# Performance work log

Hardware: AMD Instinct MI355X
Metric: run time of the kernel (lower is better)

The kernel has to match this reference:

```python
import jax, jax.numpy as jnp
import numpy as np

NUM_POINTS = 1_000_000
WINDOW = 8                      # 2^3 corner stencil for linear shape functions in 3D
GRID = (128, 128, 128)
NUM_CELLS = GRID[0] * GRID[1] * GRID[2]
CELL = 1.0 / 64.0
INV_CELL = 64.0
ORIGIN = jnp.zeros((3,), dtype=jnp.float32)
# forward_window: the 8 corner offsets of the enclosing cell
FWD_WINDOW = jnp.array([[i, j, k] for i in (0, 1) for j in (0, 1) for k in (0, 1)],
                       dtype=jnp.int32)  # [8,3]


def setup_inputs() -> dict:
    key = jax.random.key(0)
    k1, k2, k3 = jax.random.split(key, 3)
    domain = GRID[0] * CELL
    # keep particles one cell away from the boundary so all stencil hashes are in range
    pos = jax.random.uniform(k1, (NUM_POINTS, 3), dtype=jnp.float32) * (domain - 2 * CELL) + CELL
    vel = jax.random.normal(k2, (NUM_POINTS, 3), dtype=jnp.float32)
    mass = jax.random.uniform(k3, (NUM_POINTS,), dtype=jnp.float32) * 1e-3 + 1e-4
    return {"position_stack": pos, "velocity_stack": vel, "mass_stack": mass}


def reference(position_stack, velocity_stack, mass_stack):
    # ---- get_interactions: gather particle pos, hash into grid, shape functions ----
    rel = (position_stack - ORIGIN) * INV_CELL               # [N,3] position in cell units
    base = jnp.floor(rel)                                    # [N,3]
    grid_pos = base[:, None, :] + FWD_WINDOW[None, :, :].astype(rel.dtype)  # [N,8,3]
    dist = rel[:, None, :] - grid_pos                        # [N,8,3], each dim in (-1,1)

    gp = grid_pos.astype(jnp.int32)
    # get_hash, dim==3: pos[2] + pos[0]*grid[2] + pos[1]*grid[2]*grid[0]
    intr_hash = gp[..., 2] + gp[..., 0] * GRID[2] + gp[..., 1] * (GRID[2] * GRID[0])  # [N,8]

    # linear shape function: N = prod_d (1 - |x_d|); grad scaled by inv_cell_size
    w = 1.0 - jnp.abs(dist)                                  # [N,8,3]
    shapef = w[..., 0] * w[..., 1] * w[..., 2]               # [N,8]
    valid = (intr_hash >= 0) & (intr_hash < NUM_CELLS)
    shapef = jnp.where(valid, shapef, 0.0)

    g0 = -jnp.sign(dist[..., 0]) * w[..., 1] * w[..., 2]
    g1 = -jnp.sign(dist[..., 1]) * w[..., 0] * w[..., 2]
    g2 = -jnp.sign(dist[..., 2]) * w[..., 0] * w[..., 1]
    shapef_grad = jnp.stack([g0, g1, g2], axis=-1) * INV_CELL  # [N,8,3]
    shapef_grad = jnp.where(valid[..., None], shapef_grad, 0.0)

    # intr_dist_padded = -dist * cell_size (kept implicitly via dist; used in APIC-style p2g)
    # ---- p2g scatter (vmap_intr_scatter semantics): mass & momentum to grid nodes ----
    h_flat = jnp.clip(intr_hash, 0, NUM_CELLS - 1).reshape(-1)  # [N*8]
    sm = shapef * mass_stack[:, None]                           # [N,8]
    node_mass = jax.ops.segment_sum(sm.reshape(-1), h_flat, num_segments=NUM_CELLS)   # [C]
    mom = sm[..., None] * velocity_stack[:, None, :]            # [N,8,3]
    node_mom = jax.ops.segment_sum(mom.reshape(-1, 3), h_flat, num_segments=NUM_CELLS)  # [C,3]

    return jnp.concatenate([node_mass[:, None], node_mom], axis=1)  # [C,4]
```

## Files before the change

### kernel.cpp

```cpp
#include <hip/hip_runtime.h>
#include <hip/hip_fp16.h>


#define GRID_DIM   128
#define NUM_CELLS  (GRID_DIM * GRID_DIM * GRID_DIM)
#define INV_CELL   64.0f
#define OVF_MAX    65536
#define SCAN_BLKS  2048

#define TDIM       16
#define NTILES     (TDIM * TDIM * TDIM)
#define TCAP       512
#define TCNT_STR   16
#define MAXCAP     3
#define NSC        729
#define PLANE      736

__device__ __forceinline__ int cell_id(int ix, int iy, int iz) {
    return iz + ix * GRID_DIM + iy * (GRID_DIM * GRID_DIM);
}

__device__ __forceinline__ unsigned int q16(float f) {
    int q = (int)(f * 65536.0f + 0.5f);
    return (unsigned int)min(q, 65535);
}
__device__ __forceinline__ unsigned int f2h(float f) {
    return (unsigned int)__half_as_ushort(__float2half(f));
}
__device__ __forceinline__ float h2f(unsigned int b) {
    return __half2float(__ushort_as_half((unsigned short)(b & 0xffffu)));
}

__global__ __launch_bounds__(256) void tile_place_kernel(
    const float* __restrict__ pos, const float* __restrict__ vel,
    const float* __restrict__ mass, unsigned int* __restrict__ tile_cnt,
    uint4* __restrict__ lists, int* __restrict__ ovf_cnt,
    int* __restrict__ ovf_list, int n)
{
    int i = blockIdx.x * 256 + threadIdx.x;
    if (i >= n) return;
    float rx = pos[3 * i + 0] * INV_CELL;
    float ry = pos[3 * i + 1] * INV_CELL;
    float rz = pos[3 * i + 2] * INV_CELL;
    float bx = floorf(rx), by = floorf(ry), bz = floorf(rz);
    float fx = rx - bx, fy = ry - by, fz = rz - bz;
    int ix = min(max((int)bx, 0), GRID_DIM - 1);
    int iy = min(max((int)by, 0), GRID_DIM - 1);
    int iz = min(max((int)bz, 0), GRID_DIM - 1);
    int tile = (iz >> 3) + ((ix >> 3) << 4) + ((iy >> 3) << 8);
    unsigned int s = atomicAdd(&tile_cnt[tile * TCNT_STR], 1u);
    if (s < (unsigned int)TCAP) {
        unsigned int lid = (unsigned int)((iz & 7) | ((ix & 7) << 3)
                                                   | ((iy & 7) << 6));
        uint4 r;
        r.x = q16(fx) | (q16(fy) << 16);
        r.y = q16(fz) | (f2h(mass[i]) << 16);
        r.z = f2h(vel[3 * i + 0]) | (f2h(vel[3 * i + 1]) << 16);
        r.w = f2h(vel[3 * i + 2]) | (lid << 16);
        lists[(size_t)tile * TCAP + (int)s] = r;
    } else {
        int o = atomicAdd(ovf_cnt, 1);
        if (o < OVF_MAX) ovf_list[o] = i;
    }
}

__global__ __launch_bounds__(512) void tile_gather_kernel(
    const uint4* __restrict__ lists, const unsigned int* __restrict__ tile_cnt,
    float4* __restrict__ out)
{
    __shared__ unsigned int cnt_s[NSC];
    __shared__ unsigned int rec_s[4 * MAXCAP * PLANE];
    __shared__ float nacc[4 * 512];

    int tid = threadIdx.x;
    int swz = (blockIdx.x & 7) * 512 + (blockIdx.x >> 3);
    int bz = swz & 15;
    int bx = (swz >> 4) & 15;
    int by = swz >> 8;
    int g0x = bx * 8, g0y = by * 8, g0z = bz * 8;

    for (int sc = tid; sc < NSC; sc += 512) cnt_s[sc] = 0;
    nacc[tid] = 0.0f; nacc[512 + tid] = 0.0f;
    nacc[1024 + tid] = 0.0f; nacc[1536 + tid] = 0.0f;
    __syncthreads();

    #pragma unroll
    for (int dty = -1; dty <= 0; ++dty)
    #pragma unroll
    for (int dtx = -1; dtx <= 0; ++dtx)
    #pragma unroll
    for (int dtz = -1; dtz <= 0; ++dtz) {
        int tx_ = bx + dtx, ty_ = by + dty, tz_ = bz + dtz;
        if ((tx_ < 0) || (ty_ < 0) || (tz_ < 0)) continue;
        int tile = tz_ + (tx_ << 4) + (ty_ << 8);
        int cnt = (int)min(tile_cnt[tile * TCNT_STR], (unsigned int)TCAP);
        const uint4* base = lists + (size_t)tile * TCAP;
        int c0x = tx_ * 8, c0y = ty_ * 8, c0z = tz_ * 8;
        for (int r = tid; r < cnt; r += 512) {
            uint4 rec = base[r];
            unsigned int lid = rec.w >> 16;
            int cz = c0z + (int)(lid & 7u);
            int cx = c0x + (int)((lid >> 3) & 7u);
            int cy = c0y + (int)(lid >> 6);
            int uz = cz - (g0z - 1), ux = cx - (g0x - 1), uy = cy - (g0y - 1);
            if (((unsigned)uz < 9u) & ((unsigned)ux < 9u) & ((unsigned)uy < 9u)) {
                int sc = uy * 81 + ux * 9 + uz;
                unsigned int j = atomicAdd(&cnt_s[sc], 1u);
                if (j < MAXCAP) {
                    rec_s[(0 * MAXCAP + j) * PLANE + sc] = rec.x;
                    rec_s[(1 * MAXCAP + j) * PLANE + sc] = rec.y;
                    rec_s[(2 * MAXCAP + j) * PLANE + sc] = rec.z;
                    rec_s[(3 * MAXCAP + j) * PLANE + sc] = rec.w;
                } else {
                    float fx = (float)(rec.x & 0xffffu) * (1.0f / 65536.0f);
                    float fy = (float)(rec.x >> 16)     * (1.0f / 65536.0f);
                    float fz = (float)(rec.y & 0xffffu) * (1.0f / 65536.0f);
                    float m  = h2f(rec.y >> 16);
                    float vx = h2f(rec.z), vy = h2f(rec.z >> 16), vz = h2f(rec.w);
                    #pragma unroll
                    for (int oy = 0; oy < 2; ++oy)
                    #pragma unroll
                    for (int ox = 0; ox < 2; ++ox)
                    #pragma unroll
                    for (int oz = 0; oz < 2; ++oz) {
                        int pz = cz + oz - g0z;
                        int px = cx + ox - g0x;
                        int py = cy + oy - g0y;
                        if (((unsigned)pz < 8u) & ((unsigned)px < 8u) &
                            ((unsigned)py < 8u)) {
                            float w = (ox ? fx : 1.0f - fx) *
                                      (oy ? fy : 1.0f - fy) *
                                      (oz ? fz : 1.0f - fz);
                            float sm = w * m;
                            int idx = py * 64 + px * 8 + pz;
                            atomicAdd(&nacc[0 * 512 + idx], sm);
                            atomicAdd(&nacc[1 * 512 + idx], sm * vx);
                            atomicAdd(&nacc[2 * 512 + idx], sm * vy);
                            atomicAdd(&nacc[3 * 512 + idx], sm * vz);
                        }
                    }
                }
            }
        }
    }
    __syncthreads();

    int tz = tid & 7, tx = (tid >> 3) & 7, ty = tid >> 6;
    float a0 = nacc[tid], a1 = nacc[512 + tid];
    float a2 = nacc[1024 + tid], a3 = nacc[1536 + tid];

    #pragma unroll
    for (int dy = 0; dy < 2; ++dy) {
        #pragma unroll
        for (int dx = 0; dx < 2; ++dx) {
            int scb = (ty + dy) * 81 + (tx + dx) * 9 + tz;
            #pragma unroll
            for (int dz = 0; dz < 2; ++dz) {
                int sc = scb + dz;
                int cnt = min((int)cnt_s[sc], MAXCAP);
                for (int j = 0; j < cnt; ++j) {
                    unsigned r0 = rec_s[(0 * MAXCAP + j) * PLANE + sc];
                    unsigned r1 = rec_s[(1 * MAXCAP + j) * PLANE + sc];
                    unsigned r2 = rec_s[(2 * MAXCAP + j) * PLANE + sc];
                    unsigned r3 = rec_s[(3 * MAXCAP + j) * PLANE + sc];
                    float fx = (float)(r0 & 0xffffu) * (1.0f / 65536.0f);
                    float fy = (float)(r0 >> 16)     * (1.0f / 65536.0f);
                    float fz = (float)(r1 & 0xffffu) * (1.0f / 65536.0f);
                    float wx = dx ? (1.0f - fx) : fx;
                    float wy = dy ? (1.0f - fy) : fy;
                    float wz = dz ? (1.0f - fz) : fz;
                    float sm = wx * wy * wz * h2f(r1 >> 16);
                    a0 += sm;
                    a1 += sm * h2f(r2);
                    a2 += sm * h2f(r2 >> 16);
                    a3 += sm * h2f(r3);
                }
            }
        }
    }
    int id = (g0z + tz) + (g0x + tx) * GRID_DIM
           + (g0y + ty) * (GRID_DIM * GRID_DIM);
    out[id] = make_float4(a0, a1, a2, a3);
}

__global__ __launch_bounds__(256) void fixup_kernel(
    const float* __restrict__ pos, const float* __restrict__ vel,
    const float* __restrict__ mass, const int* __restrict__ ovf_cnt,
    const int* __restrict__ ovf_list, float* __restrict__ out)
{
    int total = min(*ovf_cnt, OVF_MAX);
    for (int k = blockIdx.x * 256 + threadIdx.x; k < total; k += gridDim.x * 256) {
        int i = ovf_list[k];
        float px = pos[3 * i + 0] * INV_CELL;
        float py = pos[3 * i + 1] * INV_CELL;
        float pz = pos[3 * i + 2] * INV_CELL;
        float bx = floorf(px), by = floorf(py), bz = floorf(pz);
        float fx = px - bx, fy = py - by, fz = pz - bz;
        int ix = (int)bx, iy = (int)by, iz = (int)bz;
        float m = mass[i];
        float vx = vel[3 * i + 0], vy = vel[3 * i + 1], vz = vel[3 * i + 2];
        float wx[2] = { 1.0f - fx, fx }, wy[2] = { 1.0f - fy, fy }, wz[2] = { 1.0f - fz, fz };
        #pragma unroll
        for (int a = 0; a < 2; ++a)
            #pragma unroll
            for (int b = 0; b < 2; ++b)
                #pragma unroll
                for (int c = 0; c < 2; ++c) {
                    int h = cell_id(ix + a, iy + b, iz + c);
                    bool valid = (h >= 0) && (h < NUM_CELLS);
                    int hc = min(max(h, 0), NUM_CELLS - 1);
                    float s = valid ? (wx[a] * wy[b] * wz[c]) : 0.0f;
                    float sm = s * m;
                    float* cell = out + 4 * (size_t)hc;
                    atomicAdd(cell + 0, sm);
                    atomicAdd(cell + 1, sm * vx);
                    atomicAdd(cell + 2, sm * vy);
                    atomicAdd(cell + 3, sm * vz);
                }
    }
}

__global__ __launch_bounds__(256) void s_hist_kernel(
    const float* __restrict__ pos, int* __restrict__ counts, int n)
{
    int i = blockIdx.x * 256 + threadIdx.x;
    if (i >= n) return;
    int ix = min(max((int)floorf(pos[3 * i + 0] * INV_CELL), 0), GRID_DIM - 1);
    int iy = min(max((int)floorf(pos[3 * i + 1] * INV_CELL), 0), GRID_DIM - 1);
    int iz = min(max((int)floorf(pos[3 * i + 2] * INV_CELL), 0), GRID_DIM - 1);
    atomicAdd(&counts[cell_id(ix, iy, iz)], 1);
}

__global__ __launch_bounds__(256) void s_scan_partials_kernel(
    const int* __restrict__ counts, int* __restrict__ partials)
{
    __shared__ int red[256];
    int t = threadIdx.x;
    int4 v = ((const int4*)counts)[blockIdx.x * 256 + t];
    red[t] = v.x + v.y + v.z + v.w;
    __syncthreads();
    for (int off = 128; off > 0; off >>= 1) {
        if (t < off) red[t] += red[t + off];
        __syncthreads();
    }
    if (t == 0) partials[blockIdx.x] = red[0];
}

__global__ __launch_bounds__(1024) void s_scan_tops_kernel(int* __restrict__ partials)
{
    __shared__ int s[1024];
    int t = threadIdx.x;
    int p0 = partials[2 * t], p1 = partials[2 * t + 1];
    int sum = p0 + p1;
    s[t] = sum;
    __syncthreads();
    for (int off = 1; off < 1024; off <<= 1) {
        int x = (t >= off) ? s[t - off] : 0;
        __syncthreads();
        s[t] += x;
        __syncthreads();
    }
    int excl = s[t] - sum;
    partials[2 * t] = excl;
    partials[2 * t + 1] = excl + p0;
}

__global__ __launch_bounds__(256) void s_scan_final_kernel(
    const int* __restrict__ counts, const int* __restrict__ partials,
    int* __restrict__ offsets, int* __restrict__ cursors)
{
    __shared__ int s[256];
    int t = threadIdx.x;
    int g = blockIdx.x * 256 + t;
    int4 v = ((const int4*)counts)[g];
    int sum = v.x + v.y + v.z + v.w;
    s[t] = sum;
    __syncthreads();
    for (int off = 1; off < 256; off <<= 1) {
        int x = (t >= off) ? s[t - off] : 0;
        __syncthreads();
        s[t] += x;
        __syncthreads();
    }
    int run = partials[blockIdx.x] + s[t] - sum;
    int4 o = make_int4(run, run + v.x, run + v.x + v.y, run + v.x + v.y + v.z);
    ((int4*)offsets)[g] = o;
    ((int4*)cursors)[g] = o;
}

__global__ __launch_bounds__(256) void s_binplace_kernel(
    const float* __restrict__ pos, const float* __restrict__ vel,
    const float* __restrict__ mass, int* __restrict__ cursors,
    float4* __restrict__ records, int n)
{
    int i = blockIdx.x * 256 + threadIdx.x;
    if (i >= n) return;
    float rx = pos[3 * i + 0] * INV_CELL;
    float ry = pos[3 * i + 1] * INV_CELL;
    float rz = pos[3 * i + 2] * INV_CELL;
    int ix = min(max((int)floorf(rx), 0), GRID_DIM - 1);
    int iy = min(max((int)floorf(ry), 0), GRID_DIM - 1);
    int iz = min(max((int)floorf(rz), 0), GRID_DIM - 1);
    int slot = atomicAdd(&cursors[cell_id(ix, iy, iz)], 1);
    records[2 * slot + 0] = make_float4(rx, ry, rz, mass[i]);
    records[2 * slot + 1] = make_float4(vel[3 * i + 0], vel[3 * i + 1],
                                        vel[3 * i + 2], 0.0f);
}

__global__ __launch_bounds__(256) void s_node_gather_kernel(
    const float4* __restrict__ records, const int* __restrict__ offsets,
    const int* __restrict__ cursors, float4* __restrict__ out)
{
    int id = blockIdx.x * 256 + threadIdx.x;
    int gz = id & (GRID_DIM - 1);
    int gx = (id >> 7) & (GRID_DIM - 1);
    int gy = id >> 14;
    float fgx = (float)gx, fgy = (float)gy, fgz = (float)gz;
    float a0 = 0.0f, a1 = 0.0f, a2 = 0.0f, a3 = 0.0f;
    int z0 = max(gz - 1, 0), y0 = max(gy - 1, 0), x0 = max(gx - 1, 0);
    for (int cy = y0; cy <= gy; ++cy) {
        for (int cx = x0; cx <= gx; ++cx) {
            int cb = cx * GRID_DIM + cy * (GRID_DIM * GRID_DIM);
            int beg = offsets[cb + z0];
            int end = cursors[cb + gz];
            for (int p = beg; p < end; ++p) {
                float4 r0 = records[2 * p + 0];
                float4 r1 = records[2 * p + 1];
                float w = (1.0f - fabsf(r0.x - fgx)) *
                          (1.0f - fabsf(r0.y - fgy)) *
                          (1.0f - fabsf(r0.z - fgz));
                float sm = w * r0.w;
                a0 += sm; a1 += sm * r1.x; a2 += sm * r1.y; a3 += sm * r1.z;
            }
        }
    }
    out[id] = make_float4(a0, a1, a2, a3);
}

__global__ __launch_bounds__(256) void p2g_scatter_kernel(
    const float* __restrict__ pos, const float* __restrict__ vel,
    const float* __restrict__ mass, float* __restrict__ out, int n)
{
    int i = blockIdx.x * blockDim.x + threadIdx.x;
    if (i >= n) return;
    float px = pos[3 * i + 0] * INV_CELL;
    float py = pos[3 * i + 1] * INV_CELL;
    float pz = pos[3 * i + 2] * INV_CELL;
    float bx = floorf(px), by = floorf(py), bz = floorf(pz);
    float fx = px - bx, fy = py - by, fz = pz - bz;
    int ix = (int)bx, iy = (int)by, iz = (int)bz;
    float m = mass[i];
    float vx = vel[3 * i + 0], vy = vel[3 * i + 1], vz = vel[3 * i + 2];
    float wx[2] = { 1.0f - fx, fx }, wy[2] = { 1.0f - fy, fy }, wz[2] = { 1.0f - fz, fz };
    #pragma unroll
    for (int a = 0; a < 2; ++a)
        #pragma unroll
        for (int b = 0; b < 2; ++b)
            #pragma unroll
            for (int c = 0; c < 2; ++c) {
                int h = cell_id(ix + a, iy + b, iz + c);
                bool valid = (h >= 0) && (h < NUM_CELLS);
                int hc = min(max(h, 0), NUM_CELLS - 1);
                float s = valid ? (wx[a] * wy[b] * wz[c]) : 0.0f;
                float sm = s * m;
                float* cell = out + 4 * (size_t)hc;
                atomicAdd(cell + 0, sm);
                atomicAdd(cell + 1, sm * vx);
                atomicAdd(cell + 2, sm * vy);
                atomicAdd(cell + 3, sm * vz);
            }
}

extern "C" void kernel_launch(void* const* d_in, const int* in_sizes, int n_in,
                              void* d_out, int out_size, void* d_ws, size_t ws_size,
                              hipStream_t stream) {
    const float* pos  = (const float*)d_in[0];
    const float* vel  = (const float*)d_in[1];
    const float* mass = (const float*)d_in[2];
    float* out = (float*)d_out;
    int n = in_sizes[2];
    int blocks = (n + 255) / 256;

    size_t t_off_lists = (size_t)NTILES * TCNT_STR * 4;
    size_t t_off_ovf   = t_off_lists + (size_t)NTILES * TCAP * 16;
    size_t need_tiles  = t_off_ovf + 256 + (size_t)OVF_MAX * 4;

    size_t s_off_offsets  = (size_t)NUM_CELLS * 4;
    size_t s_off_records  = s_off_offsets + (size_t)NUM_CELLS * 4;
    size_t s_off_partials = s_off_records + (size_t)n * 32;
    size_t need_sorted    = s_off_partials + (size_t)SCAN_BLKS * 4;

    if (ws_size >= need_tiles) {
        char* ws = (char*)d_ws;
        unsigned int* tile_cnt = (unsigned int*)ws;
        uint4* lists  = (uint4*)(ws + t_off_lists);
        int* ovf_cnt  = (int*)(ws + t_off_ovf);
        int* ovf_list = ovf_cnt + 64;

        hipMemsetAsync(tile_cnt, 0, t_off_lists, stream);
        hipMemsetAsync(ovf_cnt, 0, 4, stream);
        tile_place_kernel<<<blocks, 256, 0, stream>>>(
            pos, vel, mass, tile_cnt, lists, ovf_cnt, ovf_list, n);
        tile_gather_kernel<<<NTILES, 512, 0, stream>>>(
            lists, tile_cnt, (float4*)out);
        fixup_kernel<<<32, 256, 0, stream>>>(pos, vel, mass, ovf_cnt,
                                             ovf_list, out);
    } else if (ws_size >= need_sorted) {
        char* ws = (char*)d_ws;
        int* counts   = (int*)ws;
        int* offsets  = (int*)(ws + s_off_offsets);
        float4* records = (float4*)(ws + s_off_records);
        int* partials = (int*)(ws + s_off_partials);

        hipMemsetAsync(counts, 0, (size_t)NUM_CELLS * 4, stream);
        s_hist_kernel<<<blocks, 256, 0, stream>>>(pos, counts, n);
        s_scan_partials_kernel<<<SCAN_BLKS, 256, 0, stream>>>(counts, partials);
        s_scan_tops_kernel<<<1, 1024, 0, stream>>>(partials);
        s_scan_final_kernel<<<SCAN_BLKS, 256, 0, stream>>>(counts, partials,
                                                           offsets, counts);
        s_binplace_kernel<<<blocks, 256, 0, stream>>>(pos, vel, mass, counts,
                                                      records, n);
        s_node_gather_kernel<<<NUM_CELLS / 256, 256, 0, stream>>>(
            records, offsets, counts, (float4*)out);
    } else {
        hipMemsetAsync(out, 0, (size_t)out_size * sizeof(float), stream);
        p2g_scatter_kernel<<<blocks, 256, 0, stream>>>(pos, vel, mass, out, n);
    }
}
```

Before: 173.3 us.

## Split tile bins per XCD to localize counter atomics and flatten gather

Each tile's particle bin is split into 8 sub-bins keyed by the placing block's XCD, so the global atomic counters for a sub-bin are hit only by blocks on one XCD. The gather kernel builds a prefix sum over the 64 sub-segments (8 neighbour tiles times 8 XCDs) and walks them with a flat thread loop using a binary search. The change also adds nontemporal loads and stores and loads velocity and mass only when a particle fits in its bin. Per-sub-bin capacity drops to 48, which may send more particles to the slower overflow fixup path.

```diff
diff --git a/kernel.cpp b/kernel.cpp
--- a/kernel.cpp
+++ b/kernel.cpp
@@ -10,12 +10,14 @@
 
 #define TDIM       16
 #define NTILES     (TDIM * TDIM * TDIM)
-#define TCAP       512
-#define TCNT_STR   16
+#define NXCD       8
+#define XCAP       48
 #define MAXCAP     3
 #define NSC        729
 #define PLANE      736
 
+typedef float floatx4 __attribute__((ext_vector_type(4)));
+
 __device__ __forceinline__ int cell_id(int ix, int iy, int iz) {
     return iz + ix * GRID_DIM + iy * (GRID_DIM * GRID_DIM);
 }
@@ -31,7 +33,7 @@
     return __half2float(__ushort_as_half((unsigned short)(b & 0xffffu)));
 }
 
-__global__ __launch_bounds__(256) void tile_place_kernel(
+__global__ __launch_bounds__(256) void xcd_place_kernel(
     const float* __restrict__ pos, const float* __restrict__ vel,
     const float* __restrict__ mass, unsigned int* __restrict__ tile_cnt,
     uint4* __restrict__ lists, int* __restrict__ ovf_cnt,
@@ -39,38 +41,47 @@
 {
     int i = blockIdx.x * 256 + threadIdx.x;
     if (i >= n) return;
-    float rx = pos[3 * i + 0] * INV_CELL;
-    float ry = pos[3 * i + 1] * INV_CELL;
-    float rz = pos[3 * i + 2] * INV_CELL;
+    int xcd = blockIdx.x & (NXCD - 1);
+    float px = __builtin_nontemporal_load(&pos[3 * i + 0]);
+    float py = __builtin_nontemporal_load(&pos[3 * i + 1]);
+    float pz = __builtin_nontemporal_load(&pos[3 * i + 2]);
+    float rx = px * INV_CELL, ry = py * INV_CELL, rz = pz * INV_CELL;
     float bx = floorf(rx), by = floorf(ry), bz = floorf(rz);
     float fx = rx - bx, fy = ry - by, fz = rz - bz;
     int ix = min(max((int)bx, 0), GRID_DIM - 1);
     int iy = min(max((int)by, 0), GRID_DIM - 1);
     int iz = min(max((int)bz, 0), GRID_DIM - 1);
-    int tile = (iz >> 3) + ((ix >> 3) << 4) + ((iy >> 3) << 8);
-    unsigned int s = atomicAdd(&tile_cnt[tile * TCNT_STR], 1u);
-    if (s < (unsigned int)TCAP) {
+    int tile = (iz >> 3) | ((ix >> 3) << 4) | ((iy >> 3) << 8);
+    int sub = (xcd << 12) | tile;
+    unsigned int s = atomicAdd(&tile_cnt[sub], 1u);
+    if (s < (unsigned int)XCAP) {
+        float m  = __builtin_nontemporal_load(&mass[i]);
+        float vx = __builtin_nontemporal_load(&vel[3 * i + 0]);
+        float vy = __builtin_nontemporal_load(&vel[3 * i + 1]);
+        float vz = __builtin_nontemporal_load(&vel[3 * i + 2]);
         unsigned int lid = (unsigned int)((iz & 7) | ((ix & 7) << 3)
                                                    | ((iy & 7) << 6));
         uint4 r;
         r.x = q16(fx) | (q16(fy) << 16);
-        r.y = q16(fz) | (f2h(mass[i]) << 16);
-        r.z = f2h(vel[3 * i + 0]) | (f2h(vel[3 * i + 1]) << 16);
-        r.w = f2h(vel[3 * i + 2]) | (lid << 16);
-        lists[(size_t)tile * TCAP + (int)s] = r;
+        r.y = q16(fz) | (f2h(m) << 16);
+        r.z = f2h(vx) | (f2h(vy) << 16);
+        r.w = f2h(vz) | (lid << 16);
+        lists[(size_t)sub * XCAP + (int)s] = r;
     } else {
         int o = atomicAdd(ovf_cnt, 1);
         if (o < OVF_MAX) ovf_list[o] = i;
     }
 }
 
-__global__ __launch_bounds__(512) void tile_gather_kernel(
+__global__ __launch_bounds__(512) void xcd_gather_kernel(
     const uint4* __restrict__ lists, const unsigned int* __restrict__ tile_cnt,
     float4* __restrict__ out)
 {
     __shared__ unsigned int cnt_s[NSC];
     __shared__ unsigned int rec_s[4 * MAXCAP * PLANE];
     __shared__ float nacc[4 * 512];
+    __shared__ unsigned int seg_off[65];
+    __shared__ unsigned int seg_cnt[64];
 
     int tid = threadIdx.x;
     int swz = (blockIdx.x & 7) * 512 + (blockIdx.x >> 3);
@@ -82,62 +93,77 @@
     for (int sc = tid; sc < NSC; sc += 512) cnt_s[sc] = 0;
     nacc[tid] = 0.0f; nacc[512 + tid] = 0.0f;
     nacc[1024 + tid] = 0.0f; nacc[1536 + tid] = 0.0f;
-    __syncthreads();
-
-    #pragma unroll
-    for (int dty = -1; dty <= 0; ++dty)
-    #pragma unroll
-    for (int dtx = -1; dtx <= 0; ++dtx)
-    #pragma unroll
-    for (int dtz = -1; dtz <= 0; ++dtz) {
-        int tx_ = bx + dtx, ty_ = by + dty, tz_ = bz + dtz;
-        if ((tx_ < 0) || (ty_ < 0) || (tz_ < 0)) continue;
+
+    if (tid < 64) {
+        int xcd = tid & 7, lt = tid >> 3;
+        int ltz = lt & 1, ltx = (lt >> 1) & 1, lty = lt >> 2;
+        int tz_ = bz - 1 + ltz, tx_ = bx - 1 + ltx, ty_ = by - 1 + lty;
+        unsigned int c = 0;
+        if ((tz_ >= 0) & (tx_ >= 0) & (ty_ >= 0)) {
+            int tile = tz_ + (tx_ << 4) + (ty_ << 8);
+            c = min(tile_cnt[(xcd << 12) | tile], (unsigned int)XCAP);
+        }
+        seg_cnt[tid] = c;
+    }
+    __syncthreads();
+    if (tid == 0) {
+        unsigned int run = 0;
+        for (int s = 0; s < 64; ++s) { seg_off[s] = run; run += seg_cnt[s]; }
+        seg_off[64] = run;
+    }
+    __syncthreads();
+    int R = (int)seg_off[64];
+
+    for (int r = tid; r < R; r += 512) {
+        int s = 0;
+        #pragma unroll
+        for (int step = 32; step >= 1; step >>= 1)
+            if (seg_off[s + step] <= (unsigned int)r) s += step;
+        int xcd = s & 7, lt = s >> 3;
+        int ltz = lt & 1, ltx = (lt >> 1) & 1, lty = lt >> 2;
+        int tz_ = bz - 1 + ltz, tx_ = bx - 1 + ltx, ty_ = by - 1 + lty;
         int tile = tz_ + (tx_ << 4) + (ty_ << 8);
-        int cnt = (int)min(tile_cnt[tile * TCNT_STR], (unsigned int)TCAP);
-        const uint4* base = lists + (size_t)tile * TCAP;
-        int c0x = tx_ * 8, c0y = ty_ * 8, c0z = tz_ * 8;
-        for (int r = tid; r < cnt; r += 512) {
-            uint4 rec = base[r];
-            unsigned int lid = rec.w >> 16;
-            int cz = c0z + (int)(lid & 7u);
-            int cx = c0x + (int)((lid >> 3) & 7u);
-            int cy = c0y + (int)(lid >> 6);
-            int uz = cz - (g0z - 1), ux = cx - (g0x - 1), uy = cy - (g0y - 1);
-            if (((unsigned)uz < 9u) & ((unsigned)ux < 9u) & ((unsigned)uy < 9u)) {
-                int sc = uy * 81 + ux * 9 + uz;
-                unsigned int j = atomicAdd(&cnt_s[sc], 1u);
-                if (j < MAXCAP) {
-                    rec_s[(0 * MAXCAP + j) * PLANE + sc] = rec.x;
-                    rec_s[(1 * MAXCAP + j) * PLANE + sc] = rec.y;
-                    rec_s[(2 * MAXCAP + j) * PLANE + sc] = rec.z;
-                    rec_s[(3 * MAXCAP + j) * PLANE + sc] = rec.w;
-                } else {
-                    float fx = (float)(rec.x & 0xffffu) * (1.0f / 65536.0f);
-                    float fy = (float)(rec.x >> 16)     * (1.0f / 65536.0f);
-                    float fz = (float)(rec.y & 0xffffu) * (1.0f / 65536.0f);
-                    float m  = h2f(rec.y >> 16);
-                    float vx = h2f(rec.z), vy = h2f(rec.z >> 16), vz = h2f(rec.w);
-                    #pragma unroll
-                    for (int oy = 0; oy < 2; ++oy)
-                    #pragma unroll
-                    for (int ox = 0; ox < 2; ++ox)
-                    #pragma unroll
-                    for (int oz = 0; oz < 2; ++oz) {
-                        int pz = cz + oz - g0z;
-                        int px = cx + ox - g0x;
-                        int py = cy + oy - g0y;
-                        if (((unsigned)pz < 8u) & ((unsigned)px < 8u) &
-                            ((unsigned)py < 8u)) {
-                            float w = (ox ? fx : 1.0f - fx) *
-                                      (oy ? fy : 1.0f - fy) *
-                                      (oz ? fz : 1.0f - fz);
-                            float sm = w * m;
-                            int idx = py * 64 + px * 8 + pz;
-                            atomicAdd(&nacc[0 * 512 + idx], sm);
-                            atomicAdd(&nacc[1 * 512 + idx], sm * vx);
-                            atomicAdd(&nacc[2 * 512 + idx], sm * vy);
-                            atomicAdd(&nacc[3 * 512 + idx], sm * vz);
-                        }
+        int j = r - (int)seg_off[s];
+        uint4 rec = lists[(size_t)((xcd << 12) | tile) * XCAP + j];
+        unsigned int lid = rec.w >> 16;
+        int cz = tz_ * 8 + (int)(lid & 7u);
+        int cx = tx_ * 8 + (int)((lid >> 3) & 7u);
+        int cy = ty_ * 8 + (int)(lid >> 6);
+        int uz = cz - (g0z - 1), ux = cx - (g0x - 1), uy = cy - (g0y - 1);
+        if (((unsigned)uz < 9u) & ((unsigned)ux < 9u) & ((unsigned)uy < 9u)) {
+            int sc = uy * 81 + ux * 9 + uz;
+            unsigned int j2 = atomicAdd(&cnt_s[sc], 1u);
+            if (j2 < MAXCAP) {
+                rec_s[(0 * MAXCAP + j2) * PLANE + sc] = rec.x;
+                rec_s[(1 * MAXCAP + j2) * PLANE + sc] = rec.y;
+                rec_s[(2 * MAXCAP + j2) * PLANE + sc] = rec.z;
+                rec_s[(3 * MAXCAP + j2) * PLANE + sc] = rec.w;
+            } else {
+                float fx = (float)(rec.x & 0xffffu) * (1.0f / 65536.0f);
+                float fy = (float)(rec.x >> 16)     * (1.0f / 65536.0f);
+                float fz = (float)(rec.y & 0xffffu) * (1.0f / 65536.0f);
+                float m  = h2f(rec.y >> 16);
+                float vx = h2f(rec.z), vy = h2f(rec.z >> 16), vz = h2f(rec.w);
+                #pragma unroll
+                for (int oy = 0; oy < 2; ++oy)
+                #pragma unroll
+                for (int ox = 0; ox < 2; ++ox)
+                #pragma unroll
+                for (int oz = 0; oz < 2; ++oz) {
+                    int pz = cz + oz - g0z;
+                    int px = cx + ox - g0x;
+                    int py = cy + oy - g0y;
+                    if (((unsigned)pz < 8u) & ((unsigned)px < 8u) &
+                        ((unsigned)py < 8u)) {
+                        float w = (ox ? fx : 1.0f - fx) *
+                                  (oy ? fy : 1.0f - fy) *
+                                  (oz ? fz : 1.0f - fz);
+                        float sm = w * m;
+                        int idx = py * 64 + px * 8 + pz;
+                        atomicAdd(&nacc[0 * 512 + idx], sm);
+                        atomicAdd(&nacc[1 * 512 + idx], sm * vx);
+                        atomicAdd(&nacc[2 * 512 + idx], sm * vy);
+                        atomicAdd(&nacc[3 * 512 + idx], sm * vz);
                     }
                 }
             }
@@ -180,7 +206,8 @@
     }
     int id = (g0z + tz) + (g0x + tx) * GRID_DIM
            + (g0y + ty) * (GRID_DIM * GRID_DIM);
-    out[id] = make_float4(a0, a1, a2, a3);
+    floatx4 v = { a0, a1, a2, a3 };
+    __builtin_nontemporal_store(v, (floatx4*)&out[id]);
 }
 
 __global__ __launch_bounds__(256) void fixup_kernel(
@@ -381,27 +408,27 @@
     int n = in_sizes[2];
     int blocks = (n + 255) / 256;
 
-    size_t t_off_lists = (size_t)NTILES * TCNT_STR * 4;
-    size_t t_off_ovf   = t_off_lists + (size_t)NTILES * TCAP * 16;
-    size_t need_tiles  = t_off_ovf + 256 + (size_t)OVF_MAX * 4;
+    size_t x_off_lists = (size_t)NXCD * NTILES * 4;
+    size_t x_off_ovf   = x_off_lists + (size_t)NXCD * NTILES * XCAP * 16;
+    size_t need_xcd    = x_off_ovf + 256 + (size_t)OVF_MAX * 4;
 
     size_t s_off_offsets  = (size_t)NUM_CELLS * 4;
     size_t s_off_records  = s_off_offsets + (size_t)NUM_CELLS * 4;
     size_t s_off_partials = s_off_records + (size_t)n * 32;
     size_t need_sorted    = s_off_partials + (size_t)SCAN_BLKS * 4;
 
-    if (ws_size >= need_tiles) {
+    if (ws_size >= need_xcd) {
         char* ws = (char*)d_ws;
         unsigned int* tile_cnt = (unsigned int*)ws;
-        uint4* lists  = (uint4*)(ws + t_off_lists);
-        int* ovf_cnt  = (int*)(ws + t_off_ovf);
+        uint4* lists  = (uint4*)(ws + x_off_lists);
+        int* ovf_cnt  = (int*)(ws + x_off_ovf);
         int* ovf_list = ovf_cnt + 64;
 
-        hipMemsetAsync(tile_cnt, 0, t_off_lists, stream);
-        hipMemsetAsync(ovf_cnt, 0, 4, stream);
-        tile_place_kernel<<<blocks, 256, 0, stream>>>(
+        (void)hipMemsetAsync(tile_cnt, 0, x_off_lists, stream);
+        (void)hipMemsetAsync(ovf_cnt, 0, 4, stream);
+        xcd_place_kernel<<<blocks, 256, 0, stream>>>(
             pos, vel, mass, tile_cnt, lists, ovf_cnt, ovf_list, n);
-        tile_gather_kernel<<<NTILES, 512, 0, stream>>>(
+        xcd_gather_kernel<<<NTILES, 512, 0, stream>>>(
             lists, tile_cnt, (float4*)out);
         fixup_kernel<<<32, 256, 0, stream>>>(pos, vel, mass, ovf_cnt,
                                              ovf_list, out);
@@ -412,7 +439,7 @@
         float4* records = (float4*)(ws + s_off_records);
         int* partials = (int*)(ws + s_off_partials);
 
-        hipMemsetAsync(counts, 0, (size_t)NUM_CELLS * 4, stream);
+        (void)hipMemsetAsync(counts, 0, (size_t)NUM_CELLS * 4, stream);
         s_hist_kernel<<<blocks, 256, 0, stream>>>(pos, counts, n);
         s_scan_partials_kernel<<<SCAN_BLKS, 256, 0, stream>>>(counts, partials);
         s_scan_tops_kernel<<<1, 1024, 0, stream>>>(partials);
@@ -423,7 +450,7 @@
         s_node_gather_kernel<<<NUM_CELLS / 256, 256, 0, stream>>>(
             records, offsets, counts, (float4*)out);
     } else {
-        hipMemsetAsync(out, 0, (size_t)out_size * sizeof(float), stream);
+        (void)hipMemsetAsync(out, 0, (size_t)out_size * sizeof(float), stream);
         p2g_scatter_kernel<<<blocks, 256, 0, stream>>>(pos, vel, mass, out, n);
     }
 }
```

After: 179.7 us. 3.7% more time.
